# Optimization experiments

Hardware: AMD Instinct MI355X
Metric: run time of the kernel (lower is better)

Reference implementation:

```python
import jax, jax.numpy as jnp
import numpy as np

NEG_SLOPE = 0.2


def gat_conv(h, src, dst, n_dst, W_src, W_dst, attn_l, attn_r, bias):
    # h: [N_src, F_in]; edges src->dst; dst nodes are a prefix of src nodes.
    H, D = attn_l.shape
    z_src = (h @ W_src).reshape(h.shape[0], H, D)          # [N_src, H, D]
    z_dst = (h[:n_dst] @ W_dst).reshape(n_dst, H, D)       # [N_dst, H, D]
    el = jnp.einsum('nhd,hd->nh', z_src, attn_l)           # [N_src, H]
    er = jnp.einsum('nhd,hd->nh', z_dst, attn_r)           # [N_dst, H]
    e = jax.nn.leaky_relu(el[src] + er[dst], NEG_SLOPE)    # [E, H]
    # numerically stable edge softmax over incoming edges of each dst node
    m = jax.ops.segment_max(e, dst, num_segments=n_dst)    # [N_dst, H]
    w = jnp.exp(e - m[dst])                                # [E, H]
    s = jax.ops.segment_sum(w, dst, num_segments=n_dst)    # [N_dst, H]
    alpha = w / s[dst]                                     # [E, H]
    msg = alpha[:, :, None] * z_src[src]                   # [E, H, D]
    out = jax.ops.segment_sum(msg, dst, num_segments=n_dst)
    return out + bias                                      # [N_dst, H, D]


def setup_inputs() -> dict:
    key = jax.random.key(0)
    ks = jax.random.split(key, 16)
    IN, HID, HEADS, NCLS = 256, 64, 4, 47
    N_SRC0, N_DST0, E0 = 200000, 50000, 500000
    N_DST1, E1 = 10000, 100000
    sc0 = 0.1
    inp = {
        'x': jax.random.normal(ks[0], (N_SRC0, IN), jnp.float32),
        'src0': jax.random.randint(ks[1], (E0,), 0, N_SRC0, jnp.int32),
        'dst0': jax.random.randint(ks[2], (E0,), 0, N_DST0, jnp.int32),
        'src1': jax.random.randint(ks[3], (E1,), 0, N_DST0, jnp.int32),
        'dst1': jax.random.randint(ks[4], (E1,), 0, N_DST1, jnp.int32),
        'num_dst0': N_DST0,
        'num_dst1': N_DST1,
        'W0_src': jax.random.normal(ks[5], (IN, HEADS * HID), jnp.float32) * sc0,
        'W0_dst': jax.random.normal(ks[6], (IN, HEADS * HID), jnp.float32) * sc0,
        'attn_l0': jax.random.normal(ks[7], (HEADS, HID), jnp.float32) * sc0,
        'attn_r0': jax.random.normal(ks[8], (HEADS, HID), jnp.float32) * sc0,
        'bias0': jnp.zeros((HEADS, HID), jnp.float32),
        'W1_src': jax.random.normal(ks[9], (HEADS * HID, HEADS * NCLS), jnp.float32) * sc0,
        'W1_dst': jax.random.normal(ks[10], (HEADS * HID, HEADS * NCLS), jnp.float32) * sc0,
        'attn_l1': jax.random.normal(ks[11], (HEADS, NCLS), jnp.float32) * sc0,
        'attn_r1': jax.random.normal(ks[12], (HEADS, NCLS), jnp.float32) * sc0,
        'bias1': jnp.zeros((HEADS, NCLS), jnp.float32),
    }
    return inp


def reference(x, src0, dst0, src1, dst1, num_dst0, num_dst1,
              W0_src, W0_dst, attn_l0, attn_r0, bias0,
              W1_src, W1_dst, attn_l1, attn_r1, bias1):
    # layer 0: GATConv + relu activation, flatten heads
    h = gat_conv(x, src0, dst0, num_dst0, W0_src, W0_dst, attn_l0, attn_r0, bias0)
    h = jax.nn.relu(h).reshape(num_dst0, -1)               # [N_dst0, H*HID]
    # layer 1: GATConv, no activation
    h = gat_conv(h, src1, dst1, num_dst1, W1_src, W1_dst, attn_l1, attn_r1, bias1)
    h = h.mean(axis=1)                                     # mean over heads -> [N_dst1, n_classes]
    return jax.nn.log_softmax(h, axis=-1)
```

## Files before the change

### kernel.cpp

```cpp
#include <hip/hip_runtime.h>
#include <math.h>

typedef _Float16 half8 __attribute__((ext_vector_type(8)));
typedef _Float16 half4 __attribute__((ext_vector_type(4)));
typedef float f32x4 __attribute__((ext_vector_type(4)));

constexpr int IN    = 256;
constexpr int NCLS  = 47;
constexpr int HD1   = 188;
constexpr float NEG_SLOPE = 0.2f;
constexpr int ND0 = 50000, ND1 = 10000;

static __device__ __forceinline__ float leaky(float x) {
    return x >= 0.f ? x : NEG_SLOPE * x;
}

__device__ __forceinline__ void gload16(const void* g, void* l) {
    __builtin_amdgcn_global_load_lds((const __attribute__((address_space(1))) void*)g,
                                     (__attribute__((address_space(3))) void*)l, 16, 0, 0);
}

__global__ __launch_bounds__(256) void prep_k(
        const float* __restrict__ W0s, const float* __restrict__ W1s,
        const float* __restrict__ W0d, const float* __restrict__ W1d,
        const float* __restrict__ al0, const float* __restrict__ ar0,
        const float* __restrict__ al1, const float* __restrict__ ar1,
        _Float16* __restrict__ B0t, _Float16* __restrict__ B1t,
        float* __restrict__ vl0T, float* __restrict__ vr0T,
        float* __restrict__ vl1T, float* __restrict__ vr1T) {
    int b = blockIdx.x, t = threadIdx.x;
    if (b < 256) {
        int id = b * 256 + t;
        int n = id >> 8, k = id & 255;
        int dst = n * 256 + ((((k >> 3) ^ (n & 31)) & 31) << 3) + (k & 7);
        B0t[dst] = (_Float16)W0s[(size_t)k * 256 + n];
    } else if (b < 448) {
        int id = (b - 256) * 256 + t;
        int n = id >> 8, k = id & 255;
        int dst = n * 256 + ((((k >> 3) ^ (n & 31)) & 31) << 3) + (k & 7);
        B1t[dst] = (n < HD1) ? (_Float16)W1s[(size_t)k * HD1 + n] : (_Float16)0.f;
    } else if (b == 448) {
        for (int i = t; i < 1024; i += 256) {
            int h = i >> 8, k = i & 255;
            float s = 0.f;
            for (int d = 0; d < 64; ++d)
                s += W0d[(size_t)k * 256 + h * 64 + d] * ar0[h * 64 + d];
            vr0T[h * 256 + k] = s;
        }
    } else if (b == 449) {
        for (int i = t; i < 1024; i += 256) {
            int h = i >> 8, k = i & 255;
            float s = 0.f;
            for (int d = 0; d < 64; ++d)
                s += W0s[(size_t)k * 256 + h * 64 + d] * al0[h * 64 + d];
            vl0T[h * 256 + k] = s;
        }
    } else if (b == 450) {
        for (int i = t; i < 1024; i += 256) {
            int h = i >> 8, k = i & 255;
            float s = 0.f;
            for (int d = 0; d < NCLS; ++d)
                s += W1s[(size_t)k * HD1 + h * NCLS + d] * al1[h * NCLS + d];
            vl1T[h * 256 + k] = s;
        }
    } else {
        for (int i = t; i < 1024; i += 256) {
            int h = i >> 8, k = i & 255;
            float s = 0.f;
            for (int d = 0; d < NCLS; ++d)
                s += W1d[(size_t)k * HD1 + h * NCLS + d] * ar1[h * NCLS + d];
            vr1T[h * 256 + k] = s;
        }
    }
}

__global__ __launch_bounds__(256) void cvt_lr(const float* __restrict__ x,
        const float* __restrict__ vlT, const float* __restrict__ vrT,
        _Float16* __restrict__ xh, float* __restrict__ el, float* __restrict__ er,
        int M, int Mr) {
    int wv = threadIdx.x >> 6, lane = threadIdx.x & 63;
    int row = blockIdx.x * 4 + wv;
    if (row >= M) return;
    float4 xa = *(const float4*)(x + (size_t)row * IN + lane * 4);
    half4 hv;
    hv[0] = (_Float16)xa.x; hv[1] = (_Float16)xa.y;
    hv[2] = (_Float16)xa.z; hv[3] = (_Float16)xa.w;
    *(half4*)(xh + (size_t)row * IN + lane * 4) = hv;
    float sl[4], sr[4];
    bool do_r = row < Mr;
#pragma unroll
    for (int h = 0; h < 4; ++h) {
        float4 v = *(const float4*)(vlT + h * IN + lane * 4);
        sl[h] = xa.x * v.x + xa.y * v.y + xa.z * v.z + xa.w * v.w;
        float4 u = *(const float4*)(vrT + h * IN + lane * 4);
        sr[h] = xa.x * u.x + xa.y * u.y + xa.z * u.z + xa.w * u.w;
    }
#pragma unroll
    for (int off = 32; off; off >>= 1)
#pragma unroll
        for (int h = 0; h < 4; ++h) {
            sl[h] += __shfl_xor(sl[h], off);
            sr[h] += __shfl_xor(sr[h], off);
        }
    if (lane == 0) {
        *(float4*)(el + (size_t)row * 4) = make_float4(sl[0], sl[1], sl[2], sl[3]);
        if (do_r)
            *(float4*)(er + (size_t)row * 4) = make_float4(sr[0], sr[1], sr[2], sr[3]);
    }
}

template <int NCOLS>
__global__ __launch_bounds__(512, 2) void gemmw(const _Float16* __restrict__ Ah,
        const _Float16* __restrict__ BtS, _Float16* __restrict__ Z, int M, int ntiles) {
    constexpr int NCF = NCOLS / 16;
    __shared__ __align__(16) _Float16 Bs[NCOLS * 256];
    const int t = threadIdx.x, l = t & 63, w = t >> 6;
    const int lr = l & 15, lh = l >> 4;
    constexpr int BI = (NCOLS * 256 * 2) / (512 * 16);
#pragma unroll
    for (int it = 0; it < BI; ++it) {
        int c = it * 512 + t;
        gload16(BtS + c * 8, (char*)Bs + c * 16);
    }
    __syncthreads();

    const int NW = gridDim.x * 8;
    const int gw = blockIdx.x * 8 + w;

    half8 p0[8], p1[8];

    auto issue = [&](int tile, half8 (&p)[8]) {
        int row = tile * 16 + lr; if (row >= M) row = M - 1;
        const _Float16* ap = Ah + (size_t)row * 256 + lh * 8;
#pragma unroll
        for (int ks = 0; ks < 8; ++ks) p[ks] = *(const half8*)(ap + ks * 32);
        __builtin_amdgcn_sched_barrier(0);
    };

    auto compute = [&](int tile, half8 (&p)[8]) {
        f32x4 acc[NCF];
#pragma unroll
        for (int cf = 0; cf < NCF; ++cf) {
            acc[cf][0] = 0.f; acc[cf][1] = 0.f; acc[cf][2] = 0.f; acc[cf][3] = 0.f;
        }
#pragma unroll
        for (int ks = 0; ks < 8; ++ks) {
#pragma unroll
            for (int cf = 0; cf < NCF; ++cf) {
                int colr = cf * 16 + lr;
                half8 bf = *(const half8*)&Bs[colr * 256 +
                                              ((((ks * 4 + lh) ^ (colr & 31)) & 31) << 3)];
                acc[cf] = __builtin_amdgcn_mfma_f32_16x16x32_f16(p[ks], bf, acc[cf], 0, 0, 0);
            }
        }
#pragma unroll
        for (int r = 0; r < 4; ++r) {
            int xrow = tile * 16 + lh * 4 + r;
            if (xrow < M) {
#pragma unroll
                for (int cf = 0; cf < NCF; ++cf)
                    Z[(size_t)xrow * NCOLS + cf * 16 + lr] = (_Float16)acc[cf][r];
            }
        }
    };

    if (gw < ntiles) issue(gw, p0);
    for (int tt = gw; tt < ntiles; tt += 2 * NW) {
        int t1 = tt + NW;
        if (t1 < ntiles) {
            issue(t1, p1);
            asm volatile("s_waitcnt vmcnt(8)" ::: "memory");
        } else {
            asm volatile("s_waitcnt vmcnt(0)" ::: "memory");
        }
        compute(tt, p0);
        if (t1 < ntiles) {
            int t2 = tt + 2 * NW;
            if (t2 < ntiles) {
                issue(t2, p0);
                asm volatile("s_waitcnt vmcnt(8)" ::: "memory");
            } else {
                asm volatile("s_waitcnt vmcnt(0)" ::: "memory");
            }
            compute(t1, p1);
        }
    }
}

__global__ __launch_bounds__(256) void gemv_lr_f16(const _Float16* __restrict__ A,
        const float* __restrict__ vlT, const float* __restrict__ vrT,
        float* __restrict__ el, float* __restrict__ er, int M, int Mr) {
    int wv = threadIdx.x >> 6, lane = threadIdx.x & 63;
    int row = blockIdx.x * 4 + wv;
    if (row >= M) return;
    half4 ah = *(const half4*)(A + (size_t)row * IN + lane * 4);
    float a0 = (float)ah[0], a1 = (float)ah[1], a2 = (float)ah[2], a3 = (float)ah[3];
    float sl[4], sr[4];
#pragma unroll
    for (int h = 0; h < 4; ++h) {
        float4 v = *(const float4*)(vlT + h * IN + lane * 4);
        sl[h] = a0 * v.x + a1 * v.y + a2 * v.z + a3 * v.w;
        float4 u = *(const float4*)(vrT + h * IN + lane * 4);
        sr[h] = a0 * u.x + a1 * u.y + a2 * u.z + a3 * u.w;
    }
#pragma unroll
    for (int off = 32; off; off >>= 1)
#pragma unroll
        for (int h = 0; h < 4; ++h) {
            sl[h] += __shfl_xor(sl[h], off);
            sr[h] += __shfl_xor(sr[h], off);
        }
    if (lane == 0) {
        *(float4*)(el + (size_t)row * 4) = make_float4(sl[0], sl[1], sl[2], sl[3]);
        if (row < Mr)
            *(float4*)(er + (size_t)row * 4) = make_float4(sr[0], sr[1], sr[2], sr[3]);
    }
}

__global__ void hist2_k(const int* __restrict__ dst0, int E0,
                        const int* __restrict__ dst1, int E1, int* __restrict__ counts) {
    int i = blockIdx.x * blockDim.x + threadIdx.x;
    if (i < E0) atomicAdd(&counts[dst0[i]], 1);
    else if (i < E0 + E1) atomicAdd(&counts[ND0 + dst1[i - E0]], 1);
}

__global__ __launch_bounds__(256) void scan1_k(const int* __restrict__ counts, int n,
                                               int* __restrict__ part) {
    __shared__ int ws[4];
    int i = blockIdx.x * 256 + threadIdx.x;
    int lane = threadIdx.x & 63, wv = threadIdx.x >> 6;
    int s = (i < n) ? counts[i] : 0;
#pragma unroll
    for (int off = 32; off; off >>= 1) s += __shfl_xor(s, off);
    if (lane == 0) ws[wv] = s;
    __syncthreads();
    if (threadIdx.x == 0) part[blockIdx.x] = ws[0] + ws[1] + ws[2] + ws[3];
}

__global__ __launch_bounds__(256) void scan2_k(int* __restrict__ part, int nb) {
    __shared__ int ws[4];
    int tid = threadIdx.x, lane = tid & 63, wv = tid >> 6;
    int v = (tid < nb) ? part[tid] : 0;
    int x = v;
#pragma unroll
    for (int off = 1; off < 64; off <<= 1) {
        int u = __shfl_up(x, off);
        if (lane >= off) x += u;
    }
    if (lane == 63) ws[wv] = x;
    __syncthreads();
    int base = 0;
    for (int k = 0; k < wv; ++k) base += ws[k];
    if (tid < nb) part[tid] = base + x - v;
}

__global__ __launch_bounds__(256) void scan3_k(const int* __restrict__ counts, int n,
        const int* __restrict__ part, int* __restrict__ offsets, int* __restrict__ cursor) {
    __shared__ int ws[4];
    int i = blockIdx.x * 256 + threadIdx.x;
    int lane = threadIdx.x & 63, wv = threadIdx.x >> 6;
    int v = (i < n) ? counts[i] : 0;
    int x = v;
#pragma unroll
    for (int off = 1; off < 64; off <<= 1) {
        int u = __shfl_up(x, off);
        if (lane >= off) x += u;
    }
    if (lane == 63) ws[wv] = x;
    __syncthreads();
    int base = part[blockIdx.x];
    for (int k = 0; k < wv; ++k) base += ws[k];
    int off_ = base + x - v;
    if (i < n) { offsets[i] = off_; cursor[i] = off_; }
    if (i == n - 1) offsets[n] = off_ + v;
}

__global__ void scatter2_k(const int* __restrict__ src0, const int* __restrict__ dst0, int E0,
                           const int* __restrict__ src1, const int* __restrict__ dst1, int E1,
                           int* __restrict__ cursor, int* __restrict__ ssrc) {
    int i = blockIdx.x * blockDim.x + threadIdx.x;
    if (i < E0) {
        int p = atomicAdd(&cursor[dst0[i]], 1);
        ssrc[p] = src0[i];
    } else if (i < E0 + E1) {
        int j = i - E0;
        int p = atomicAdd(&cursor[ND0 + dst1[j]], 1);
        ssrc[p] = src1[j];
    }
}

__global__ __launch_bounds__(256) void agg_l0(const int* __restrict__ ssrc,
        const int* __restrict__ offs, const float* __restrict__ el,
        const float* __restrict__ er, const _Float16* __restrict__ z,
        const float* __restrict__ bias, _Float16* __restrict__ h, int nd) {
    int wv = threadIdx.x >> 6, lane = threadIdx.x & 63;
    int d = blockIdx.x * 4 + wv;
    if (d >= nd) return;
    int head = lane >> 4;
    int beg = offs[d], end = offs[d + 1];
    float erh = er[(size_t)d * 4 + head];
    float ax = 0, ay = 0, az = 0, aw = 0, ssum = 0;
    for (int j0 = beg; j0 < end; j0 += 64) {
        int nn = min(64, end - j0);
        int myidx = (lane < nn) ? ssrc[j0 + lane] : 0;
        int j = 0;
        for (; j + 4 <= nn; j += 4) {
            int s0 = __shfl(myidx, j),     s1 = __shfl(myidx, j + 1);
            int s2 = __shfl(myidx, j + 2), s3 = __shfl(myidx, j + 3);
            float e0 = el[(size_t)s0 * 4 + head], e1 = el[(size_t)s1 * 4 + head];
            float e2 = el[(size_t)s2 * 4 + head], e3 = el[(size_t)s3 * 4 + head];
            half4 zv0 = *(const half4*)(z + (size_t)s0 * 256 + lane * 4);
            half4 zv1 = *(const half4*)(z + (size_t)s1 * 256 + lane * 4);
            half4 zv2 = *(const half4*)(z + (size_t)s2 * 256 + lane * 4);
            half4 zv3 = *(const half4*)(z + (size_t)s3 * 256 + lane * 4);
            float w0 = __expf(leaky(e0 + erh)), w1 = __expf(leaky(e1 + erh));
            float w2 = __expf(leaky(e2 + erh)), w3 = __expf(leaky(e3 + erh));
            ssum += (w0 + w1) + (w2 + w3);
            ax += w0 * (float)zv0[0] + w1 * (float)zv1[0] + w2 * (float)zv2[0] + w3 * (float)zv3[0];
            ay += w0 * (float)zv0[1] + w1 * (float)zv1[1] + w2 * (float)zv2[1] + w3 * (float)zv3[1];
            az += w0 * (float)zv0[2] + w1 * (float)zv1[2] + w2 * (float)zv2[2] + w3 * (float)zv3[2];
            aw += w0 * (float)zv0[3] + w1 * (float)zv1[3] + w2 * (float)zv2[3] + w3 * (float)zv3[3];
        }
        for (; j < nn; ++j) {
            int s = __shfl(myidx, j);
            float e = el[(size_t)s * 4 + head] + erh;
            float wgt = __expf(leaky(e));
            ssum += wgt;
            half4 zv = *(const half4*)(z + (size_t)s * 256 + lane * 4);
            ax += wgt * (float)zv[0]; ay += wgt * (float)zv[1];
            az += wgt * (float)zv[2]; aw += wgt * (float)zv[3];
        }
    }
    float inv = ssum > 0.f ? 1.f / ssum : 0.f;
    const float* b = bias + lane * 4;
    half4 o;
    o[0] = (_Float16)fmaxf(ax * inv + b[0], 0.f);
    o[1] = (_Float16)fmaxf(ay * inv + b[1], 0.f);
    o[2] = (_Float16)fmaxf(az * inv + b[2], 0.f);
    o[3] = (_Float16)fmaxf(aw * inv + b[3], 0.f);
    *(half4*)(h + (size_t)d * 256 + lane * 4) = o;
}

__global__ __launch_bounds__(256) void agg_l1f(const int* __restrict__ ssrc,
        const int* __restrict__ offs, const float* __restrict__ el,
        const float* __restrict__ er, const _Float16* __restrict__ z,
        const float* __restrict__ bias, float* __restrict__ y, int nd) {
    __shared__ float ro[4][192];
    int wv = threadIdx.x >> 6, lane = threadIdx.x & 63;
    int d = blockIdx.x * 4 + wv;
    if (d >= nd) return;
    int beg = offs[ND0 + d], end = offs[ND0 + d + 1];
    float4 er4 = *(const float4*)(er + (size_t)d * 4);
    const int f0 = lane, f1 = lane + 64, f2 = lane + 128;
    const int h0 = f0 / NCLS, h1 = f1 / NCLS;
    const bool has2 = f2 < HD1;
    const int h2 = has2 ? f2 / NCLS : 3;
    float a0 = 0, a1 = 0, a2 = 0;
    float s0 = 0, s1 = 0, s2 = 0, s3 = 0;
    for (int j0 = beg; j0 < end; j0 += 64) {
        int nn = min(64, end - j0);
        int myidx = (lane < nn) ? ssrc[j0 + lane] : 0;
        int j = 0;
        for (; j + 2 <= nn; j += 2) {
            int sa_ = __shfl(myidx, j), sb_ = __shfl(myidx, j + 1);
            float4 ea = *(const float4*)(el + (size_t)sa_ * 4);
            float4 eb = *(const float4*)(el + (size_t)sb_ * 4);
            const _Float16* za = z + (size_t)sa_ * 192;
            const _Float16* zb = z + (size_t)sb_ * 192;
            float za0 = (float)za[f0], za1 = (float)za[f1], za2 = has2 ? (float)za[f2] : 0.f;
            float zb0 = (float)zb[f0], zb1 = (float)zb[f1], zb2 = has2 ? (float)zb[f2] : 0.f;
            float wa0 = __expf(leaky(ea.x + er4.x)), wa1 = __expf(leaky(ea.y + er4.y));
            float wa2 = __expf(leaky(ea.z + er4.z)), wa3 = __expf(leaky(ea.w + er4.w));
            float wb0 = __expf(leaky(eb.x + er4.x)), wb1 = __expf(leaky(eb.y + er4.y));
            float wb2 = __expf(leaky(eb.z + er4.z)), wb3 = __expf(leaky(eb.w + er4.w));
            s0 += wa0 + wb0; s1 += wa1 + wb1; s2 += wa2 + wb2; s3 += wa3 + wb3;
            a0 += (h0 == 0 ? wa0 : h0 == 1 ? wa1 : h0 == 2 ? wa2 : wa3) * za0
                + (h0 == 0 ? wb0 : h0 == 1 ? wb1 : h0 == 2 ? wb2 : wb3) * zb0;
            a1 += (h1 == 0 ? wa0 : h1 == 1 ? wa1 : h1 == 2 ? wa2 : wa3) * za1
                + (h1 == 0 ? wb0 : h1 == 1 ? wb1 : h1 == 2 ? wb2 : wb3) * zb1;
            if (has2)
                a2 += (h2 == 0 ? wa0 : h2 == 1 ? wa1 : h2 == 2 ? wa2 : wa3) * za2
                    + (h2 == 0 ? wb0 : h2 == 1 ? wb1 : h2 == 2 ? wb2 : wb3) * zb2;
        }
        for (; j < nn; ++j) {
            int s = __shfl(myidx, j);
            float4 e4 = *(const float4*)(el + (size_t)s * 4);
            float w0 = __expf(leaky(e4.x + er4.x));
            float w1 = __expf(leaky(e4.y + er4.y));
            float w2 = __expf(leaky(e4.z + er4.z));
            float w3 = __expf(leaky(e4.w + er4.w));
            s0 += w0; s1 += w1; s2 += w2; s3 += w3;
            const _Float16* zr = z + (size_t)s * 192;
            a0 += (h0 == 0 ? w0 : h0 == 1 ? w1 : h0 == 2 ? w2 : w3) * (float)zr[f0];
            a1 += (h1 == 0 ? w0 : h1 == 1 ? w1 : h1 == 2 ? w2 : w3) * (float)zr[f1];
            if (has2) a2 += (h2 == 0 ? w0 : h2 == 1 ? w1 : h2 == 2 ? w2 : w3) * (float)zr[f2];
        }
    }
    float sa = h0 == 0 ? s0 : h0 == 1 ? s1 : h0 == 2 ? s2 : s3;
    float sb = h1 == 0 ? s0 : h1 == 1 ? s1 : h1 == 2 ? s2 : s3;
    float sc = h2 == 0 ? s0 : h2 == 1 ? s1 : h2 == 2 ? s2 : s3;
    ro[wv][f0] = a0 * (sa > 0.f ? 1.f / sa : 0.f) + bias[f0];
    ro[wv][f1] = a1 * (sb > 0.f ? 1.f / sb : 0.f) + bias[f1];
    if (has2) ro[wv][f2] = a2 * (sc > 0.f ? 1.f / sc : 0.f) + bias[f2];
    asm volatile("s_waitcnt lgkmcnt(0)" ::: "memory");
    __builtin_amdgcn_sched_barrier(0);
    float vv = 0.f, v = -INFINITY;
    if (lane < NCLS) {
        vv = 0.25f * (ro[wv][lane] + ro[wv][lane + NCLS] +
                      ro[wv][lane + 2 * NCLS] + ro[wv][lane + 3 * NCLS]);
        v = vv;
    }
    float mx = v;
#pragma unroll
    for (int off = 32; off; off >>= 1) mx = fmaxf(mx, __shfl_xor(mx, off));
    float pp = (lane < NCLS) ? __expf(vv - mx) : 0.f;
    float sum = pp;
#pragma unroll
    for (int off = 32; off; off >>= 1) sum += __shfl_xor(sum, off);
    if (lane < NCLS) y[(size_t)d * NCLS + lane] = vv - mx - logf(sum);
}

extern "C" void kernel_launch(void* const* d_in, const int* in_sizes, int n_in,
                              void* d_out, int out_size, void* d_ws, size_t ws_size,
                              hipStream_t stream) {
    const float* x    = (const float*)d_in[0];
    const int*   src0 = (const int*)d_in[1];
    const int*   dst0 = (const int*)d_in[2];
    const int*   src1 = (const int*)d_in[3];
    const int*   dst1 = (const int*)d_in[4];
    const float* W0s  = (const float*)d_in[7];
    const float* W0d  = (const float*)d_in[8];
    const float* al0  = (const float*)d_in[9];
    const float* ar0  = (const float*)d_in[10];
    const float* b0   = (const float*)d_in[11];
    const float* W1s  = (const float*)d_in[12];
    const float* W1d  = (const float*)d_in[13];
    const float* al1  = (const float*)d_in[14];
    const float* ar1  = (const float*)d_in[15];
    const float* b1   = (const float*)d_in[16];
    const int E0 = in_sizes[1], E1 = in_sizes[3];
    const int NS0 = in_sizes[0] / IN;

    char* p = (char*)d_ws;
    auto take = [&](size_t bytes) {
        char* r = p;
        p += (bytes + 255) & ~(size_t)255;
        return r;
    };
    _Float16* xh   = (_Float16*)take((size_t)NS0 * 256 * 2);
    _Float16* z0   = (_Float16*)take((size_t)NS0 * 256 * 2);
    _Float16* h    = (_Float16*)take((size_t)ND0 * 256 * 2);
    _Float16* z1   = (_Float16*)take((size_t)ND0 * 192 * 2);
    float*    el0  = (float*)take((size_t)NS0 * 4 * 4);
    float*    er0  = (float*)take((size_t)ND0 * 4 * 4);
    float*    el1  = (float*)take((size_t)ND0 * 4 * 4);
    float*    er1  = (float*)take((size_t)ND1 * 4 * 4);
    _Float16* B0t  = (_Float16*)take((size_t)256 * 256 * 2);
    _Float16* B1t  = (_Float16*)take((size_t)192 * 256 * 2);
    float*    vl0T = (float*)take(4 * 256 * 4);
    float*    vr0T = (float*)take(4 * 256 * 4);
    float*    vl1T = (float*)take(4 * 256 * 4);
    float*    vr1T = (float*)take(4 * 256 * 4);
    const int NDT = ND0 + ND1;
    int* counts = (int*)take((size_t)NDT * 4);
    int* offs   = (int*)take((size_t)(NDT + 1) * 4);
    int* cur    = (int*)take((size_t)NDT * 4);
    int* ss     = (int*)take((size_t)(E0 + E1) * 4);
    int* part   = (int*)take(256 * 4);

    const int NB = (NDT + 255) / 256;
    const int NT0 = (NS0 + 15) / 16, NT1 = (ND0 + 15) / 16;

    hipMemsetAsync(counts, 0, (size_t)NDT * 4, stream);

    prep_k<<<452, 256, 0, stream>>>(W0s, W1s, W0d, W1d, al0, ar0, al1, ar1,
                                    B0t, B1t, vl0T, vr0T, vl1T, vr1T);
    hist2_k<<<(E0 + E1 + 255) / 256, 256, 0, stream>>>(dst0, E0, dst1, E1, counts);
    scan1_k<<<NB, 256, 0, stream>>>(counts, NDT, part);
    scan2_k<<<1, 256, 0, stream>>>(part, NB);
    scan3_k<<<NB, 256, 0, stream>>>(counts, NDT, part, offs, cur);
    scatter2_k<<<(E0 + E1 + 255) / 256, 256, 0, stream>>>(src0, dst0, E0, src1, dst1, E1,
                                                          cur, ss);

    cvt_lr<<<(NS0 + 3) / 4, 256, 0, stream>>>(x, vl0T, vr0T, xh, el0, er0, NS0, ND0);
    gemmw<256><<<256, 512, 0, stream>>>(xh, B0t, z0, NS0, NT0);
    agg_l0<<<(ND0 + 3) / 4, 256, 0, stream>>>(ss, offs, el0, er0, z0, b0, h, ND0);

    gemmw<192><<<256, 512, 0, stream>>>(h, B1t, z1, ND0, NT1);
    gemv_lr_f16<<<(ND0 + 3) / 4, 256, 0, stream>>>(h, vl1T, vr1T, el1, er1, ND0, ND1);
    agg_l1f<<<(ND1 + 3) / 4, 256, 0, stream>>>(ss, offs, el1, er1, z1, b1,
                                               (float*)d_out, ND1);
}
```

Before: 358.5 us.

## Aggregate raw features before projection, then run per-head GEMMs on destination nodes

Uses linearity to reorder the GAT layers. The softmax-weighted aggregation now runs over the fp16 input features for each head, producing per-head planes, and only then multiplies by that head's weight slice. The projection GEMM therefore covers destination nodes (50k and 10k) instead of all 200k source nodes, with bias, ReLU and fp32 output fused into the GEMM epilogue. The cost is a 4x larger aggregation output (per-head planes of 256 features) plus extra plane traffic and a separate final log-softmax kernel.

```diff
diff --git a/kernel.cpp b/kernel.cpp
--- a/kernel.cpp
+++ b/kernel.cpp
@@ -25,20 +25,21 @@
         const float* __restrict__ W0d, const float* __restrict__ W1d,
         const float* __restrict__ al0, const float* __restrict__ ar0,
         const float* __restrict__ al1, const float* __restrict__ ar1,
-        _Float16* __restrict__ B0t, _Float16* __restrict__ B1t,
+        _Float16* __restrict__ B0p, _Float16* __restrict__ B1p,
         float* __restrict__ vl0T, float* __restrict__ vr0T,
         float* __restrict__ vl1T, float* __restrict__ vr1T) {
     int b = blockIdx.x, t = threadIdx.x;
     if (b < 256) {
         int id = b * 256 + t;
-        int n = id >> 8, k = id & 255;
-        int dst = n * 256 + ((((k >> 3) ^ (n & 31)) & 31) << 3) + (k & 7);
-        B0t[dst] = (_Float16)W0s[(size_t)k * 256 + n];
+        int h = id >> 14, n = (id >> 8) & 63, k = id & 255;
+        int dst = (h * 64 + n) * 256 + ((((k >> 3) ^ (n & 31)) & 31) << 3) + (k & 7);
+        B0p[dst] = (_Float16)W0s[(size_t)k * 256 + h * 64 + n];
     } else if (b < 448) {
         int id = (b - 256) * 256 + t;
-        int n = id >> 8, k = id & 255;
-        int dst = n * 256 + ((((k >> 3) ^ (n & 31)) & 31) << 3) + (k & 7);
-        B1t[dst] = (n < HD1) ? (_Float16)W1s[(size_t)k * HD1 + n] : (_Float16)0.f;
+        int np = id >> 8, k = id & 255;
+        int h = np / 48, n = np % 48;
+        int dst = np * 256 + ((((k >> 3) ^ (n & 31)) & 31) << 3) + (k & 7);
+        B1p[dst] = (n < NCLS) ? (_Float16)W1s[(size_t)k * HD1 + h * NCLS + n] : (_Float16)0.f;
     } else if (b == 448) {
         for (int i = t; i < 1024; i += 256) {
             int h = i >> 8, k = i & 255;
@@ -109,14 +110,122 @@
     }
 }
 
-template <int NCOLS>
-__global__ __launch_bounds__(512, 2) void gemmw(const _Float16* __restrict__ Ah,
-        const _Float16* __restrict__ BtS, _Float16* __restrict__ Z, int M, int ntiles) {
+__global__ __launch_bounds__(256) void gemv_lr_f16(const _Float16* __restrict__ A,
+        const float* __restrict__ vlT, const float* __restrict__ vrT,
+        float* __restrict__ el, float* __restrict__ er, int M, int Mr) {
+    int wv = threadIdx.x >> 6, lane = threadIdx.x & 63;
+    int row = blockIdx.x * 4 + wv;
+    if (row >= M) return;
+    half4 ah = *(const half4*)(A + (size_t)row * IN + lane * 4);
+    float a0 = (float)ah[0], a1 = (float)ah[1], a2 = (float)ah[2], a3 = (float)ah[3];
+    float sl[4], sr[4];
+#pragma unroll
+    for (int h = 0; h < 4; ++h) {
+        float4 v = *(const float4*)(vlT + h * IN + lane * 4);
+        sl[h] = a0 * v.x + a1 * v.y + a2 * v.z + a3 * v.w;
+        float4 u = *(const float4*)(vrT + h * IN + lane * 4);
+        sr[h] = a0 * u.x + a1 * u.y + a2 * u.z + a3 * u.w;
+    }
+#pragma unroll
+    for (int off = 32; off; off >>= 1)
+#pragma unroll
+        for (int h = 0; h < 4; ++h) {
+            sl[h] += __shfl_xor(sl[h], off);
+            sr[h] += __shfl_xor(sr[h], off);
+        }
+    if (lane == 0) {
+        *(float4*)(el + (size_t)row * 4) = make_float4(sl[0], sl[1], sl[2], sl[3]);
+        if (row < Mr)
+            *(float4*)(er + (size_t)row * 4) = make_float4(sr[0], sr[1], sr[2], sr[3]);
+    }
+}
+
+__global__ __launch_bounds__(256) void aggx(const int* __restrict__ ssrc,
+        const int* __restrict__ offs, int obase,
+        const float* __restrict__ el, const float* __restrict__ er,
+        const _Float16* __restrict__ srcF, _Float16* __restrict__ aggP,
+        size_t PS, int nd) {
+    int wv = threadIdx.x >> 6, lane = threadIdx.x & 63;
+    int d = blockIdx.x * 4 + wv;
+    if (d >= nd) return;
+    int beg = offs[obase + d], end = offs[obase + d + 1];
+    float4 er4 = *(const float4*)(er + (size_t)d * 4);
+    float erv[4] = {er4.x, er4.y, er4.z, er4.w};
+    float acc[4][4];
+#pragma unroll
+    for (int h = 0; h < 4; ++h)
+#pragma unroll
+        for (int e = 0; e < 4; ++e) acc[h][e] = 0.f;
+    float S[4] = {0.f, 0.f, 0.f, 0.f};
+    for (int j0 = beg; j0 < end; j0 += 64) {
+        int nn = min(64, end - j0);
+        int myidx = (lane < nn) ? ssrc[j0 + lane] : 0;
+        int j = 0;
+        for (; j + 2 <= nn; j += 2) {
+            int sa = __shfl(myidx, j), sb = __shfl(myidx, j + 1);
+            float4 ea = *(const float4*)(el + (size_t)sa * 4);
+            float4 eb = *(const float4*)(el + (size_t)sb * 4);
+            half4 xa = *(const half4*)(srcF + (size_t)sa * 256 + lane * 4);
+            half4 xb = *(const half4*)(srcF + (size_t)sb * 256 + lane * 4);
+            float eav[4] = {ea.x, ea.y, ea.z, ea.w};
+            float ebv[4] = {eb.x, eb.y, eb.z, eb.w};
+            float wa[4], wb[4];
+#pragma unroll
+            for (int h = 0; h < 4; ++h) {
+                wa[h] = __expf(leaky(eav[h] + erv[h]));
+                wb[h] = __expf(leaky(ebv[h] + erv[h]));
+                S[h] += wa[h] + wb[h];
+            }
+            float fa[4] = {(float)xa[0], (float)xa[1], (float)xa[2], (float)xa[3]};
+            float fb[4] = {(float)xb[0], (float)xb[1], (float)xb[2], (float)xb[3]};
+#pragma unroll
+            for (int h = 0; h < 4; ++h)
+#pragma unroll
+                for (int e = 0; e < 4; ++e)
+                    acc[h][e] += wa[h] * fa[e] + wb[h] * fb[e];
+        }
+        for (; j < nn; ++j) {
+            int s = __shfl(myidx, j);
+            float4 ea = *(const float4*)(el + (size_t)s * 4);
+            half4 xa = *(const half4*)(srcF + (size_t)s * 256 + lane * 4);
+            float eav[4] = {ea.x, ea.y, ea.z, ea.w};
+            float wa[4];
+#pragma unroll
+            for (int h = 0; h < 4; ++h) {
+                wa[h] = __expf(leaky(eav[h] + erv[h]));
+                S[h] += wa[h];
+            }
+            float fa[4] = {(float)xa[0], (float)xa[1], (float)xa[2], (float)xa[3]};
+#pragma unroll
+            for (int h = 0; h < 4; ++h)
+#pragma unroll
+                for (int e = 0; e < 4; ++e)
+                    acc[h][e] += wa[h] * fa[e];
+        }
+    }
+#pragma unroll
+    for (int h = 0; h < 4; ++h) {
+        float inv = S[h] > 0.f ? 1.f / S[h] : 0.f;
+        half4 o;
+#pragma unroll
+        for (int e = 0; e < 4; ++e) o[e] = (_Float16)(acc[h][e] * inv);
+        *(half4*)(aggP + (size_t)h * PS + (size_t)d * 256 + lane * 4) = o;
+    }
+}
+
+template <int NCOLS, int CV, bool RELU, bool F32OUT>
+__global__ __launch_bounds__(512, 2) void gemmp(const _Float16* __restrict__ Aplanes,
+        size_t APS, const _Float16* __restrict__ Bplanes, const float* __restrict__ bias,
+        void* __restrict__ Z, int zstride, int M, int ntiles) {
     constexpr int NCF = NCOLS / 16;
     __shared__ __align__(16) _Float16 Bs[NCOLS * 256];
     const int t = threadIdx.x, l = t & 63, w = t >> 6;
     const int lr = l & 15, lh = l >> 4;
-    constexpr int BI = (NCOLS * 256 * 2) / (512 * 16);
+    const int hplane = blockIdx.y;
+    const _Float16* Ah  = Aplanes + (size_t)hplane * APS;
+    const _Float16* BtS = Bplanes + (size_t)hplane * NCOLS * 256;
+
+    constexpr int BI = NCOLS / 16;
 #pragma unroll
     for (int it = 0; it < BI; ++it) {
         int c = it * 512 + t;
@@ -154,12 +263,23 @@
             }
         }
 #pragma unroll
-        for (int r = 0; r < 4; ++r) {
-            int xrow = tile * 16 + lh * 4 + r;
-            if (xrow < M) {
-#pragma unroll
-                for (int cf = 0; cf < NCF; ++cf)
-                    Z[(size_t)xrow * NCOLS + cf * 16 + lr] = (_Float16)acc[cf][r];
+        for (int cf = 0; cf < NCF; ++cf) {
+            int col = cf * 16 + lr;
+            if (col < CV) {
+                float bcol = bias[hplane * CV + col];
+#pragma unroll
+                for (int r = 0; r < 4; ++r) {
+                    int row = tile * 16 + lh * 4 + r;
+                    if (row < M) {
+                        float v = acc[cf][r] + bcol;
+                        if constexpr (RELU) v = fmaxf(v, 0.f);
+                        if constexpr (F32OUT)
+                            ((float*)Z)[(size_t)row * zstride + hplane * CV + col] = v;
+                        else
+                            ((_Float16*)Z)[(size_t)row * zstride + hplane * CV + col] =
+                                (_Float16)v;
+                    }
+                }
             }
         }
     };
@@ -184,36 +304,6 @@
             }
             compute(t1, p1);
         }
-    }
-}
-
-__global__ __launch_bounds__(256) void gemv_lr_f16(const _Float16* __restrict__ A,
-        const float* __restrict__ vlT, const float* __restrict__ vrT,
-        float* __restrict__ el, float* __restrict__ er, int M, int Mr) {
-    int wv = threadIdx.x >> 6, lane = threadIdx.x & 63;
-    int row = blockIdx.x * 4 + wv;
-    if (row >= M) return;
-    half4 ah = *(const half4*)(A + (size_t)row * IN + lane * 4);
-    float a0 = (float)ah[0], a1 = (float)ah[1], a2 = (float)ah[2], a3 = (float)ah[3];
-    float sl[4], sr[4];
-#pragma unroll
-    for (int h = 0; h < 4; ++h) {
-        float4 v = *(const float4*)(vlT + h * IN + lane * 4);
-        sl[h] = a0 * v.x + a1 * v.y + a2 * v.z + a3 * v.w;
-        float4 u = *(const float4*)(vrT + h * IN + lane * 4);
-        sr[h] = a0 * u.x + a1 * u.y + a2 * u.z + a3 * u.w;
-    }
-#pragma unroll
-    for (int off = 32; off; off >>= 1)
-#pragma unroll
-        for (int h = 0; h < 4; ++h) {
-            sl[h] += __shfl_xor(sl[h], off);
-            sr[h] += __shfl_xor(sr[h], off);
-        }
-    if (lane == 0) {
-        *(float4*)(el + (size_t)row * 4) = make_float4(sl[0], sl[1], sl[2], sl[3]);
-        if (row < Mr)
-            *(float4*)(er + (size_t)row * 4) = make_float4(sr[0], sr[1], sr[2], sr[3]);
     }
 }
 
@@ -289,135 +379,25 @@
     }
 }
 
-__global__ __launch_bounds__(256) void agg_l0(const int* __restrict__ ssrc,
-        const int* __restrict__ offs, const float* __restrict__ el,
-        const float* __restrict__ er, const _Float16* __restrict__ z,
-        const float* __restrict__ bias, _Float16* __restrict__ h, int nd) {
-    int wv = threadIdx.x >> 6, lane = threadIdx.x & 63;
-    int d = blockIdx.x * 4 + wv;
-    if (d >= nd) return;
-    int head = lane >> 4;
-    int beg = offs[d], end = offs[d + 1];
-    float erh = er[(size_t)d * 4 + head];
-    float ax = 0, ay = 0, az = 0, aw = 0, ssum = 0;
-    for (int j0 = beg; j0 < end; j0 += 64) {
-        int nn = min(64, end - j0);
-        int myidx = (lane < nn) ? ssrc[j0 + lane] : 0;
-        int j = 0;
-        for (; j + 4 <= nn; j += 4) {
-            int s0 = __shfl(myidx, j),     s1 = __shfl(myidx, j + 1);
-            int s2 = __shfl(myidx, j + 2), s3 = __shfl(myidx, j + 3);
-            float e0 = el[(size_t)s0 * 4 + head], e1 = el[(size_t)s1 * 4 + head];
-            float e2 = el[(size_t)s2 * 4 + head], e3 = el[(size_t)s3 * 4 + head];
-            half4 zv0 = *(const half4*)(z + (size_t)s0 * 256 + lane * 4);
-            half4 zv1 = *(const half4*)(z + (size_t)s1 * 256 + lane * 4);
-            half4 zv2 = *(const half4*)(z + (size_t)s2 * 256 + lane * 4);
-            half4 zv3 = *(const half4*)(z + (size_t)s3 * 256 + lane * 4);
-            float w0 = __expf(leaky(e0 + erh)), w1 = __expf(leaky(e1 + erh));
-            float w2 = __expf(leaky(e2 + erh)), w3 = __expf(leaky(e3 + erh));
-            ssum += (w0 + w1) + (w2 + w3);
-            ax += w0 * (float)zv0[0] + w1 * (float)zv1[0] + w2 * (float)zv2[0] + w3 * (float)zv3[0];
-            ay += w0 * (float)zv0[1] + w1 * (float)zv1[1] + w2 * (float)zv2[1] + w3 * (float)zv3[1];
-            az += w0 * (float)zv0[2] + w1 * (float)zv1[2] + w2 * (float)zv2[2] + w3 * (float)zv3[2];
-            aw += w0 * (float)zv0[3] + w1 * (float)zv1[3] + w2 * (float)zv2[3] + w3 * (float)zv3[3];
-        }
-        for (; j < nn; ++j) {
-            int s = __shfl(myidx, j);
-            float e = el[(size_t)s * 4 + head] + erh;
-            float wgt = __expf(leaky(e));
-            ssum += wgt;
-            half4 zv = *(const half4*)(z + (size_t)s * 256 + lane * 4);
-            ax += wgt * (float)zv[0]; ay += wgt * (float)zv[1];
-            az += wgt * (float)zv[2]; aw += wgt * (float)zv[3];
-        }
-    }
-    float inv = ssum > 0.f ? 1.f / ssum : 0.f;
-    const float* b = bias + lane * 4;
-    half4 o;
-    o[0] = (_Float16)fmaxf(ax * inv + b[0], 0.f);
-    o[1] = (_Float16)fmaxf(ay * inv + b[1], 0.f);
-    o[2] = (_Float16)fmaxf(az * inv + b[2], 0.f);
-    o[3] = (_Float16)fmaxf(aw * inv + b[3], 0.f);
-    *(half4*)(h + (size_t)d * 256 + lane * 4) = o;
-}
-
-__global__ __launch_bounds__(256) void agg_l1f(const int* __restrict__ ssrc,
-        const int* __restrict__ offs, const float* __restrict__ el,
-        const float* __restrict__ er, const _Float16* __restrict__ z,
-        const float* __restrict__ bias, float* __restrict__ y, int nd) {
-    __shared__ float ro[4][192];
-    int wv = threadIdx.x >> 6, lane = threadIdx.x & 63;
-    int d = blockIdx.x * 4 + wv;
-    if (d >= nd) return;
-    int beg = offs[ND0 + d], end = offs[ND0 + d + 1];
-    float4 er4 = *(const float4*)(er + (size_t)d * 4);
-    const int f0 = lane, f1 = lane + 64, f2 = lane + 128;
-    const int h0 = f0 / NCLS, h1 = f1 / NCLS;
-    const bool has2 = f2 < HD1;
-    const int h2 = has2 ? f2 / NCLS : 3;
-    float a0 = 0, a1 = 0, a2 = 0;
-    float s0 = 0, s1 = 0, s2 = 0, s3 = 0;
-    for (int j0 = beg; j0 < end; j0 += 64) {
-        int nn = min(64, end - j0);
-        int myidx = (lane < nn) ? ssrc[j0 + lane] : 0;
-        int j = 0;
-        for (; j + 2 <= nn; j += 2) {
-            int sa_ = __shfl(myidx, j), sb_ = __shfl(myidx, j + 1);
-            float4 ea = *(const float4*)(el + (size_t)sa_ * 4);
-            float4 eb = *(const float4*)(el + (size_t)sb_ * 4);
-            const _Float16* za = z + (size_t)sa_ * 192;
-            const _Float16* zb = z + (size_t)sb_ * 192;
-            float za0 = (float)za[f0], za1 = (float)za[f1], za2 = has2 ? (float)za[f2] : 0.f;
-            float zb0 = (float)zb[f0], zb1 = (float)zb[f1], zb2 = has2 ? (float)zb[f2] : 0.f;
-            float wa0 = __expf(leaky(ea.x + er4.x)), wa1 = __expf(leaky(ea.y + er4.y));
-            float wa2 = __expf(leaky(ea.z + er4.z)), wa3 = __expf(leaky(ea.w + er4.w));
-            float wb0 = __expf(leaky(eb.x + er4.x)), wb1 = __expf(leaky(eb.y + er4.y));
-            float wb2 = __expf(leaky(eb.z + er4.z)), wb3 = __expf(leaky(eb.w + er4.w));
-            s0 += wa0 + wb0; s1 += wa1 + wb1; s2 += wa2 + wb2; s3 += wa3 + wb3;
-            a0 += (h0 == 0 ? wa0 : h0 == 1 ? wa1 : h0 == 2 ? wa2 : wa3) * za0
-                + (h0 == 0 ? wb0 : h0 == 1 ? wb1 : h0 == 2 ? wb2 : wb3) * zb0;
-            a1 += (h1 == 0 ? wa0 : h1 == 1 ? wa1 : h1 == 2 ? wa2 : wa3) * za1
-                + (h1 == 0 ? wb0 : h1 == 1 ? wb1 : h1 == 2 ? wb2 : wb3) * zb1;
-            if (has2)
-                a2 += (h2 == 0 ? wa0 : h2 == 1 ? wa1 : h2 == 2 ? wa2 : wa3) * za2
-                    + (h2 == 0 ? wb0 : h2 == 1 ? wb1 : h2 == 2 ? wb2 : wb3) * zb2;
-        }
-        for (; j < nn; ++j) {
-            int s = __shfl(myidx, j);
-            float4 e4 = *(const float4*)(el + (size_t)s * 4);
-            float w0 = __expf(leaky(e4.x + er4.x));
-            float w1 = __expf(leaky(e4.y + er4.y));
-            float w2 = __expf(leaky(e4.z + er4.z));
-            float w3 = __expf(leaky(e4.w + er4.w));
-            s0 += w0; s1 += w1; s2 += w2; s3 += w3;
-            const _Float16* zr = z + (size_t)s * 192;
-            a0 += (h0 == 0 ? w0 : h0 == 1 ? w1 : h0 == 2 ? w2 : w3) * (float)zr[f0];
-            a1 += (h1 == 0 ? w0 : h1 == 1 ? w1 : h1 == 2 ? w2 : w3) * (float)zr[f1];
-            if (has2) a2 += (h2 == 0 ? w0 : h2 == 1 ? w1 : h2 == 2 ? w2 : w3) * (float)zr[f2];
-        }
-    }
-    float sa = h0 == 0 ? s0 : h0 == 1 ? s1 : h0 == 2 ? s2 : s3;
-    float sb = h1 == 0 ? s0 : h1 == 1 ? s1 : h1 == 2 ? s2 : s3;
-    float sc = h2 == 0 ? s0 : h2 == 1 ? s1 : h2 == 2 ? s2 : s3;
-    ro[wv][f0] = a0 * (sa > 0.f ? 1.f / sa : 0.f) + bias[f0];
-    ro[wv][f1] = a1 * (sb > 0.f ? 1.f / sb : 0.f) + bias[f1];
-    if (has2) ro[wv][f2] = a2 * (sc > 0.f ? 1.f / sc : 0.f) + bias[f2];
-    asm volatile("s_waitcnt lgkmcnt(0)" ::: "memory");
-    __builtin_amdgcn_sched_barrier(0);
+__global__ __launch_bounds__(256) void final_k(const float* __restrict__ o1,
+        float* __restrict__ y, int n) {
+    int wave = threadIdx.x >> 6, lane = threadIdx.x & 63;
+    int node = blockIdx.x * 4 + wave;
+    if (node >= n) return;
+    const float* r = o1 + (size_t)node * HD1;
     float vv = 0.f, v = -INFINITY;
     if (lane < NCLS) {
-        vv = 0.25f * (ro[wv][lane] + ro[wv][lane + NCLS] +
-                      ro[wv][lane + 2 * NCLS] + ro[wv][lane + 3 * NCLS]);
+        vv = 0.25f * (r[lane] + r[lane + NCLS] + r[lane + 2 * NCLS] + r[lane + 3 * NCLS]);
         v = vv;
     }
     float mx = v;
 #pragma unroll
     for (int off = 32; off; off >>= 1) mx = fmaxf(mx, __shfl_xor(mx, off));
-    float pp = (lane < NCLS) ? __expf(vv - mx) : 0.f;
-    float sum = pp;
+    float p = (lane < NCLS) ? __expf(vv - mx) : 0.f;
+    float sum = p;
 #pragma unroll
     for (int off = 32; off; off >>= 1) sum += __shfl_xor(sum, off);
-    if (lane < NCLS) y[(size_t)d * NCLS + lane] = vv - mx - logf(sum);
+    if (lane < NCLS) y[(size_t)node * NCLS + lane] = vv - mx - logf(sum);
 }
 
 extern "C" void kernel_launch(void* const* d_in, const int* in_sizes, int n_in,
@@ -447,20 +427,21 @@
         p += (bytes + 255) & ~(size_t)255;
         return r;
     };
-    _Float16* xh   = (_Float16*)take((size_t)NS0 * 256 * 2);
-    _Float16* z0   = (_Float16*)take((size_t)NS0 * 256 * 2);
-    _Float16* h    = (_Float16*)take((size_t)ND0 * 256 * 2);
-    _Float16* z1   = (_Float16*)take((size_t)ND0 * 192 * 2);
-    float*    el0  = (float*)take((size_t)NS0 * 4 * 4);
-    float*    er0  = (float*)take((size_t)ND0 * 4 * 4);
-    float*    el1  = (float*)take((size_t)ND0 * 4 * 4);
-    float*    er1  = (float*)take((size_t)ND1 * 4 * 4);
-    _Float16* B0t  = (_Float16*)take((size_t)256 * 256 * 2);
-    _Float16* B1t  = (_Float16*)take((size_t)192 * 256 * 2);
-    float*    vl0T = (float*)take(4 * 256 * 4);
-    float*    vr0T = (float*)take(4 * 256 * 4);
-    float*    vl1T = (float*)take(4 * 256 * 4);
-    float*    vr1T = (float*)take(4 * 256 * 4);
+    _Float16* xh    = (_Float16*)take((size_t)NS0 * 256 * 2);
+    _Float16* aggP0 = (_Float16*)take((size_t)4 * ND0 * 256 * 2);
+    _Float16* hbuf  = (_Float16*)take((size_t)ND0 * 256 * 2);
+    _Float16* aggP1 = (_Float16*)take((size_t)4 * ND1 * 256 * 2);
+    float*    o1    = (float*)take((size_t)ND1 * HD1 * 4);
+    float*    el0   = (float*)take((size_t)NS0 * 4 * 4);
+    float*    er0   = (float*)take((size_t)ND0 * 4 * 4);
+    float*    el1   = (float*)take((size_t)ND0 * 4 * 4);
+    float*    er1   = (float*)take((size_t)ND1 * 4 * 4);
+    _Float16* B0p   = (_Float16*)take((size_t)4 * 64 * 256 * 2);
+    _Float16* B1p   = (_Float16*)take((size_t)4 * 48 * 256 * 2);
+    float*    vl0T  = (float*)take(4 * 256 * 4);
+    float*    vr0T  = (float*)take(4 * 256 * 4);
+    float*    vl1T  = (float*)take(4 * 256 * 4);
+    float*    vr1T  = (float*)take(4 * 256 * 4);
     const int NDT = ND0 + ND1;
     int* counts = (int*)take((size_t)NDT * 4);
     int* offs   = (int*)take((size_t)(NDT + 1) * 4);
@@ -469,12 +450,12 @@
     int* part   = (int*)take(256 * 4);
 
     const int NB = (NDT + 255) / 256;
-    const int NT0 = (NS0 + 15) / 16, NT1 = (ND0 + 15) / 16;
+    const int NT0 = (ND0 + 15) / 16, NT1 = (ND1 + 15) / 16;
 
     hipMemsetAsync(counts, 0, (size_t)NDT * 4, stream);
 
     prep_k<<<452, 256, 0, stream>>>(W0s, W1s, W0d, W1d, al0, ar0, al1, ar1,
-                                    B0t, B1t, vl0T, vr0T, vl1T, vr1T);
+                                    B0p, B1p, vl0T, vr0T, vl1T, vr1T);
     hist2_k<<<(E0 + E1 + 255) / 256, 256, 0, stream>>>(dst0, E0, dst1, E1, counts);
     scan1_k<<<NB, 256, 0, stream>>>(counts, NDT, part);
     scan2_k<<<1, 256, 0, stream>>>(part, NB);
@@ -483,11 +464,16 @@
                                                           cur, ss);
 
     cvt_lr<<<(NS0 + 3) / 4, 256, 0, stream>>>(x, vl0T, vr0T, xh, el0, er0, NS0, ND0);
-    gemmw<256><<<256, 512, 0, stream>>>(xh, B0t, z0, NS0, NT0);
-    agg_l0<<<(ND0 + 3) / 4, 256, 0, stream>>>(ss, offs, el0, er0, z0, b0, h, ND0);
-
-    gemmw<192><<<256, 512, 0, stream>>>(h, B1t, z1, ND0, NT1);
-    gemv_lr_f16<<<(ND0 + 3) / 4, 256, 0, stream>>>(h, vl1T, vr1T, el1, er1, ND0, ND1);
-    agg_l1f<<<(ND1 + 3) / 4, 256, 0, stream>>>(ss, offs, el1, er1, z1, b1,
-                                               (float*)d_out, ND1);
-}
+    aggx<<<(ND0 + 3) / 4, 256, 0, stream>>>(ss, offs, 0, el0, er0, xh,
+                                            aggP0, (size_t)ND0 * 256, ND0);
+    gemmp<64, 64, true, false><<<dim3(128, 4), 512, 0, stream>>>(
+        aggP0, (size_t)ND0 * 256, B0p, b0, (void*)hbuf, 256, ND0, NT0);
+
+    gemv_lr_f16<<<(ND0 + 3) / 4, 256, 0, stream>>>(hbuf, vl1T, vr1T, el1, er1, ND0, ND1);
+    aggx<<<(ND1 + 3) / 4, 256, 0, stream>>>(ss, offs, ND0, el1, er1, hbuf,
+                                            aggP1, (size_t)ND1 * 256, ND1);
+    gemmp<48, 47, false, true><<<dim3(32, 4), 512, 0, stream>>>(
+        aggP1, (size_t)ND1 * 256, B1p, b1, (void*)o1, HD1, ND1, NT1);
+
+    final_k<<<(ND1 + 3) / 4, 256, 0, stream>>>(o1, (float*)d_out, ND1);
+}
```

Result: slower. 372.4 us (+3.9%).
